# Optimization experiments

Hardware: AMD Instinct MI355X
Metric: run time of the kernel (lower is better)

Reference implementation:

```python
import jax, jax.numpy as jnp
import numpy as np

B, L, H, NH = 4, 512, 512, 8
DK = H // NH
REPR_IN, REPR_HID = 53, 32
EPS = 1e-5


def setup_inputs() -> dict:
    key = jax.random.key(0)
    ks = jax.random.split(key, 12)
    x = jax.random.normal(ks[0], (B, L, H), dtype=jnp.float32)
    mask = jax.random.randint(ks[1], (B, L), 0, 2, dtype=jnp.int32)
    refCov = jax.random.normal(ks[2], (B, L, L, REPR_IN), dtype=jnp.float32)
    def lin(k, fan_in, fan_out):
        return jax.random.normal(k, (fan_in, fan_out), dtype=jnp.float32) / np.sqrt(fan_in)
    Wv = lin(ks[3], H, H); bv = jnp.zeros((H,), jnp.float32)
    W1 = lin(ks[4], REPR_IN, REPR_HID); b1 = jnp.zeros((REPR_HID,), jnp.float32)
    W2 = lin(ks[5], REPR_HID, NH); b2 = jnp.zeros((NH,), jnp.float32)
    Wo = lin(ks[6], H, H); bo = jnp.zeros((H,), jnp.float32)
    gamma = jnp.ones((H,), jnp.float32); beta = jnp.zeros((H,), jnp.float32)
    return {"x": x, "mask": mask, "refCov": refCov, "Wv": Wv, "bv": bv,
            "W1": W1, "b1": b1, "W2": W2, "b2": b2, "Wo": Wo, "bo": bo,
            "gamma": gamma, "beta": beta}


def reference(x, mask, refCov, Wv, bv, W1, b1, W2, b2, Wo, bo, gamma, beta):
    Bx, Lx, Hx = x.shape
    residual = x
    # value projection -> (B, NH, L, DK)
    value = (x @ Wv + bv).reshape(Bx, Lx, NH, DK).transpose(0, 2, 1, 3)
    # per-pair MLP on refCov: (B, L, L, 53) -> (B, L, L, NH)
    h1 = jax.nn.relu(refCov @ W1 + b1)
    scores = jnp.transpose(h1 @ W2 + b2, (0, 3, 1, 2))  # (B, NH, L, L)
    # pairwise mask and softmax
    m = mask.astype(bool)
    mask2d = m[:, :, None] & m[:, None, :]              # (B, L, L)
    masked = jnp.where(mask2d[:, None, :, :], scores, -jnp.inf)
    all_inf_rows = ~jnp.any(mask2d, axis=-1)            # (B, L) rows fully masked
    masked = jnp.where(all_inf_rows[:, None, :, None], 0.0, masked)
    attn = jax.nn.softmax(masked, axis=-1)
    # weighted sum and output projection
    out = jnp.einsum('bhij,bhjd->bhid', attn, value)
    out = out.transpose(0, 2, 1, 3).reshape(Bx, Lx, Hx)
    out = out @ Wo + bo
    # residual + LayerNorm
    y = residual + out
    mu = jnp.mean(y, axis=-1, keepdims=True)
    var = jnp.var(y, axis=-1, keepdims=True)
    return (y - mu) / jnp.sqrt(var + EPS) * gamma + beta
```

## Files before the change

### kernel.cpp

```cpp
#include <hip/hip_runtime.h>
#include <hip/hip_bf16.h>
#include <math.h>

#define B 4
#define L 512
#define H 512
#define NH 8
#define DK 64
#define RIN 53
#define RHID 32

using short8 = __attribute__((ext_vector_type(8))) short;
using ushort8v = __attribute__((ext_vector_type(8))) unsigned short;
using f32x4 = __attribute__((ext_vector_type(4))) float;

__device__ __forceinline__ float waveReduceSum(float v) {
#pragma unroll
  for (int off = 32; off > 0; off >>= 1) v += __shfl_xor(v, off, 64);
  return v;
}

__device__ __forceinline__ unsigned short cvt_bf16(float f) {
  __hip_bfloat16 h = __float2bfloat16(f);
  return __builtin_bit_cast(unsigned short, h);
}

__global__ __launch_bounds__(512) void prep_kernel(
    const int* __restrict__ mask, int* __restrict__ jidx, int* __restrict__ nv,
    const float* __restrict__ Wv, const float* __restrict__ Wo,
    unsigned short* __restrict__ WvT, unsigned short* __restrict__ WoT) {
  const int bid = blockIdx.x;
  const int tid = threadIdx.x;
  if (bid < 4) {
    const int b = bid;
    const int lane = tid & 63, wv = tid >> 6;
    __shared__ int wtot[8], woff[8];
    const int m = (mask[b * 512 + tid] != 0);
    const unsigned long long bal = __ballot(m);
    const int lpre = __popcll(bal & ((1ull << lane) - 1ull));
    if (lane == 0) wtot[wv] = __popcll(bal);
    __syncthreads();
    if (tid == 0) {
      int acc = 0;
#pragma unroll
      for (int q = 0; q < 8; ++q) {
        woff[q] = acc;
        acc += wtot[q];
      }
      nv[b] = acc;
    }
    __syncthreads();
    if (m) jidx[b * 512 + woff[wv] + lpre] = tid;
    return;
  }
  const int t = bid - 4;
  const int matsel = t >> 6;
  const int tile = t & 63;
  const float* W = matsel ? Wo : Wv;
  unsigned short* WT = matsel ? WoT : WvT;
  const int k0 = (tile & 7) * 64, n0 = (tile >> 3) * 64;
  __shared__ float sT[64][65];
  {
    const int r = tid >> 3, c0 = (tid & 7) * 8;
    const float4 v0 = *(const float4*)(W + (size_t)(k0 + r) * 512 + n0 + c0);
    const float4 v1 = *(const float4*)(W + (size_t)(k0 + r) * 512 + n0 + c0 + 4);
    sT[r][c0] = v0.x; sT[r][c0 + 1] = v0.y; sT[r][c0 + 2] = v0.z; sT[r][c0 + 3] = v0.w;
    sT[r][c0 + 4] = v1.x; sT[r][c0 + 5] = v1.y; sT[r][c0 + 6] = v1.z; sT[r][c0 + 7] = v1.w;
  }
  __syncthreads();
  {
    const int n = tid >> 3, c0 = (tid & 7) * 8;
    ushort8v o;
#pragma unroll
    for (int cc = 0; cc < 8; ++cc) o[cc] = cvt_bf16(sT[c0 + cc][n]);
    *(ushort8v*)(WT + (size_t)(n0 + n) * 512 + k0 + c0) = o;
  }
}

template <int AMODE, int OMODE>
__device__ __forceinline__ void gemm32x64(
    const void* __restrict__ Aq, int lda, const unsigned short* __restrict__ Bs,
    int ldb, const float* __restrict__ bias, void* __restrict__ Cp, int ldc) {
  __shared__ unsigned short sA[32 * 72];
  __shared__ unsigned short sB[64 * 72];
  __shared__ float sC[32][68];
  const int tid = threadIdx.x;
  const int w = tid >> 6, l = tid & 63, g = l >> 4, a = l & 15;
  const int wm = (w >> 1) * 16, wn = (w & 1) * 32;
  f32x4 acc0 = {}, acc1 = {};
  const int ar = tid >> 3, ak = (tid & 7) * 8;

  auto loadA = [&](int k0) {
    ushort8v r;
    if constexpr (AMODE == 1) {
      const float* Af = (const float*)Aq;
      const float* p = Af + (size_t)ar * lda + k0 + ak;
      const float4 v0 = *(const float4*)p;
      const float4 v1 = *(const float4*)(p + 4);
      r[0] = cvt_bf16(v0.x); r[1] = cvt_bf16(v0.y);
      r[2] = cvt_bf16(v0.z); r[3] = cvt_bf16(v0.w);
      r[4] = cvt_bf16(v1.x); r[5] = cvt_bf16(v1.y);
      r[6] = cvt_bf16(v1.z); r[7] = cvt_bf16(v1.w);
    } else {
      const unsigned short* Ab = (const unsigned short*)Aq;
      r = *(const ushort8v*)(Ab + (size_t)ar * lda + k0 + ak);
    }
    return r;
  };
  auto loadB = [&](int k0, int q) {
    const int s = tid + q * 256;
    return *(const ushort8v*)(Bs + (size_t)(s >> 3) * ldb + k0 + (s & 7) * 8);
  };

  ushort8v aR = loadA(0);
  ushort8v bR0 = loadB(0, 0), bR1 = loadB(0, 1);
  for (int k0 = 0; k0 < 512; k0 += 64) {
    *(ushort8v*)(&sA[ar * 72 + ak]) = aR;
    *(ushort8v*)(&sB[ar * 72 + ak]) = bR0;
    *(ushort8v*)(&sB[(ar + 32) * 72 + ak]) = bR1;
    __syncthreads();
    if (k0 < 448) {
      aR = loadA(k0 + 64);
      bR0 = loadB(k0 + 64, 0);
      bR1 = loadB(k0 + 64, 1);
    }
#pragma unroll
    for (int ks = 0; ks < 2; ++ks) {
      const short8 af = *(const short8*)(&sA[(wm + a) * 72 + ks * 32 + g * 8]);
      const short8 bf0 = *(const short8*)(&sB[(wn + a) * 72 + ks * 32 + g * 8]);
      const short8 bf1 =
          *(const short8*)(&sB[(wn + 16 + a) * 72 + ks * 32 + g * 8]);
      acc0 = __builtin_amdgcn_mfma_f32_16x16x32_bf16(af, bf0, acc0, 0, 0, 0);
      acc1 = __builtin_amdgcn_mfma_f32_16x16x32_bf16(af, bf1, acc1, 0, 0, 0);
    }
    __syncthreads();
  }

#pragma unroll
  for (int r = 0; r < 4; ++r) {
    sC[wm + g * 4 + r][wn + a] = acc0[r];
    sC[wm + g * 4 + r][wn + 16 + a] = acc1[r];
  }
  __syncthreads();

  if constexpr (OMODE == 2) {
    const int n = tid >> 2, iq = (tid & 3) * 8;
    const float bv = bias ? bias[n] : 0.f;
    ushort8v o;
#pragma unroll
    for (int cc = 0; cc < 8; ++cc) o[cc] = cvt_bf16(sC[iq + cc][n] + bv);
    *(ushort8v*)((unsigned short*)Cp + (size_t)n * ldc + iq) = o;
  } else {
    const int m = tid >> 3, c8 = (tid & 7) * 8;
    float v[8];
#pragma unroll
    for (int cc = 0; cc < 8; ++cc) {
      v[cc] = sC[m][c8 + cc];
      if (bias) v[cc] += bias[c8 + cc];
    }
    if constexpr (OMODE == 1) {
      ushort8v o;
#pragma unroll
      for (int cc = 0; cc < 8; ++cc) o[cc] = cvt_bf16(v[cc]);
      *(ushort8v*)((unsigned short*)Cp + (size_t)m * ldc + c8) = o;
    } else {
      *(float4*)((float*)Cp + (size_t)m * ldc + c8) =
          make_float4(v[0], v[1], v[2], v[3]);
      *(float4*)((float*)Cp + (size_t)m * ldc + c8 + 4) =
          make_float4(v[4], v[5], v[6], v[7]);
    }
  }
}

__global__ __launch_bounds__(256) void gemm_xw_t_kernel(
    const float* __restrict__ x, const unsigned short* __restrict__ WvT,
    const float* __restrict__ bv, unsigned short* __restrict__ valT) {
  const int n0 = blockIdx.x * 64;
  const int m0 = blockIdx.y * 32;
  const int b = m0 >> 9, i0 = m0 & 511;
  gemm32x64<1, 2>(x + (size_t)m0 * 512, 512, WvT + (size_t)n0 * 512, 512,
                  bv + n0, valT + (size_t)b * 262144 + (size_t)n0 * 512 + i0,
                  512);
}

__global__ __launch_bounds__(256) void attn_value_kernel(
    const unsigned short* __restrict__ attnb,
    const unsigned short* __restrict__ valT, unsigned short* __restrict__ ctx) {
  const int bid = blockIdx.x;
  const int it = bid & 15, h = (bid >> 4) & 7, b = bid >> 7;
  const int i0 = it * 32;
  gemm32x64<0, 1>(attnb + ((size_t)((b * 8 + h) * 512 + i0)) * 512, 512,
                  valT + (size_t)b * 262144 + (size_t)(h * 64) * 512, 512,
                  nullptr, ctx + ((size_t)(b * 512 + i0)) * 512 + h * 64, 512);
}

__global__ __launch_bounds__(256) void gemm_proj_kernel(
    const unsigned short* __restrict__ ctx, const unsigned short* __restrict__ WoT,
    const float* __restrict__ bo, float* __restrict__ proj) {
  const int n0 = blockIdx.x * 64;
  const int m0 = blockIdx.y * 32;
  gemm32x64<0, 0>(ctx + (size_t)m0 * 512, 512, WoT + (size_t)n0 * 512, 512,
                  bo + n0, proj + (size_t)m0 * 512 + n0, 512);
}

__global__ __launch_bounds__(256) void residual_ln_kernel(
    const float* __restrict__ x, const float* __restrict__ proj,
    const float* __restrict__ gamma, const float* __restrict__ beta,
    float* __restrict__ out) {
  const int row = blockIdx.x;
  const int tid = threadIdx.x;
  __shared__ float redS[4], redQ[4];
  float y[2];
  float ls = 0.f, lq = 0.f;
#pragma unroll
  for (int p = 0; p < 2; ++p) {
    const int c = tid + p * 256;
    const float v = x[(size_t)row * H + c] + proj[(size_t)row * H + c];
    y[p] = v;
    ls += v;
    lq += v * v;
  }
  const int lane = tid & 63, wave = tid >> 6;
  ls = waveReduceSum(ls);
  lq = waveReduceSum(lq);
  if (lane == 0) {
    redS[wave] = ls;
    redQ[wave] = lq;
  }
  __syncthreads();
  const float sum = redS[0] + redS[1] + redS[2] + redS[3];
  const float sq = redQ[0] + redQ[1] + redQ[2] + redQ[3];
  const float mu = sum * (1.f / H);
  const float var = sq * (1.f / H) - mu * mu;
  const float inv = rsqrtf(var + 1e-5f);
#pragma unroll
  for (int p = 0; p < 2; ++p) {
    const int c = tid + p * 256;
    out[(size_t)row * H + c] = (y[p] - mu) * inv * gamma[c] + beta[c];
  }
}

__global__ __launch_bounds__(256) void scores_softmax_kernel(
    const float* __restrict__ refCov, const int* __restrict__ mask,
    const int* __restrict__ jidx, const int* __restrict__ nvArr,
    const float* __restrict__ W1, const float* __restrict__ b1,
    const float* __restrict__ W2, const float* __restrict__ b2,
    unsigned short* __restrict__ attnb) {
  __shared__ unsigned short sH1[512 * 34];
  __shared__ int sJ[512];
  __shared__ float redbuf[4][16];

  const int tid = threadIdx.x;
  const int b = blockIdx.x >> 9;
  const int i = blockIdx.x & (L - 1);
  const int w = tid >> 6;
  const int l = tid & 63;
  const int g = l >> 4;
  const int a = l & 15;

  const int mi = mask[b * L + i];
  const int nv = nvArr[b];

  if (mi == 0 || nv == 0) {
    const ushort4 u4 = {0x3B00u, 0x3B00u, 0x3B00u, 0x3B00u};
#pragma unroll
    for (int q = 0; q < 4; ++q) {
      const int f4 = q * 256 + tid;
      const int h = f4 >> 7;
      const int c4 = f4 & 127;
      *(ushort4*)(attnb + ((size_t)(b * NH + h) * L + i) * L + c4 * 4) = u4;
    }
    return;
  }

  sJ[tid] = jidx[b * 512 + tid];
  sJ[tid + 256] = jidx[b * 512 + 256 + tid];

  short8 w1f[2][2];
#pragma unroll
  for (int ks = 0; ks < 2; ++ks)
#pragma unroll
    for (int nt = 0; nt < 2; ++nt)
#pragma unroll
      for (int e = 0; e < 8; ++e) {
        const int k = ks * 32 + g * 8 + e;
        w1f[ks][nt][e] =
            (k < RIN) ? (short)cvt_bf16(W1[k * RHID + nt * 16 + a]) : (short)0;
      }
  short8 w2f;
#pragma unroll
  for (int e = 0; e < 8; ++e) {
    const int k = g * 8 + e;
    w2f[e] = (a < NH) ? (short)cvt_bf16(W2[k * NH + a]) : (short)0;
  }
  const float b1v0 = b1[a];
  const float b1v1 = b1[16 + a];
  const float b2v = (a < NH) ? b2[a] : 0.f;

  __syncthreads();

  const int NT = (nv + 15) >> 4;
  f32x4 sc[8];

#pragma unroll
  for (int mt = 0; mt < 8; ++mt) {
    const int t = mt * 4 + w;
    if (t >= NT) continue;
    const int s = t * 16 + a;
    const int j = sJ[(s < nv) ? s : (nv - 1)];
    const float* rp = refCov + ((size_t)((b << 9) + i) * 512 + j) * RIN;

    const float4 u0 = *(const float4*)(rp + g * 8);
    const float4 u1 = *(const float4*)(rp + g * 8 + 4);
    const int base0 = (g < 3) ? (32 + g * 8) : 32;
    const int base1 = (g == 0) ? 36 : (g == 1) ? 44 : 49;
    const float4 v0 = *(const float4*)(rp + base0);
    const float4 v1 = *(const float4*)(rp + base1);
    float t1[8];
    if (g < 3) {
      t1[0] = v0.x; t1[1] = v0.y; t1[2] = v0.z; t1[3] = v0.w;
    } else {
      t1[0] = 0.f; t1[1] = 0.f; t1[2] = 0.f; t1[3] = 0.f;
    }
    if (g < 2) {
      t1[4] = v1.x; t1[5] = v1.y; t1[6] = v1.z; t1[7] = v1.w;
    } else if (g == 2) {
      t1[4] = v1.w;
      t1[5] = 0.f; t1[6] = 0.f; t1[7] = 0.f;
    } else {
      t1[4] = 0.f; t1[5] = 0.f; t1[6] = 0.f; t1[7] = 0.f;
    }
    short8 af0, af1;
    af0[0] = (short)cvt_bf16(u0.x); af0[1] = (short)cvt_bf16(u0.y);
    af0[2] = (short)cvt_bf16(u0.z); af0[3] = (short)cvt_bf16(u0.w);
    af0[4] = (short)cvt_bf16(u1.x); af0[5] = (short)cvt_bf16(u1.y);
    af0[6] = (short)cvt_bf16(u1.z); af0[7] = (short)cvt_bf16(u1.w);
#pragma unroll
    for (int e = 0; e < 8; ++e) af1[e] = (short)cvt_bf16(t1[e]);

    f32x4 h0 = f32x4{b1v0, b1v0, b1v0, b1v0};
    f32x4 h1v = f32x4{b1v1, b1v1, b1v1, b1v1};
    h0 = __builtin_amdgcn_mfma_f32_16x16x32_bf16(af0, w1f[0][0], h0, 0, 0, 0);
    h1v = __builtin_amdgcn_mfma_f32_16x16x32_bf16(af0, w1f[0][1], h1v, 0, 0, 0);
    h0 = __builtin_amdgcn_mfma_f32_16x16x32_bf16(af1, w1f[1][0], h0, 0, 0, 0);
    h1v = __builtin_amdgcn_mfma_f32_16x16x32_bf16(af1, w1f[1][1], h1v, 0, 0, 0);

#pragma unroll
    for (int r = 0; r < 4; ++r) {
      sH1[(t * 16 + g * 4 + r) * 34 + a] = cvt_bf16(fmaxf(h0[r], 0.f));
      sH1[(t * 16 + g * 4 + r) * 34 + 16 + a] = cvt_bf16(fmaxf(h1v[r], 0.f));
    }

    const short8 af2 = *(const short8*)(&sH1[(t * 16 + a) * 34 + g * 8]);
    f32x4 acc = f32x4{b2v, b2v, b2v, b2v};
    sc[mt] = __builtin_amdgcn_mfma_f32_16x16x32_bf16(af2, w2f, acc, 0, 0, 0);
  }

  float mx = -INFINITY;
#pragma unroll
  for (int mt = 0; mt < 8; ++mt) {
    const int t = mt * 4 + w;
    if (t >= NT) continue;
#pragma unroll
    for (int r = 0; r < 4; ++r) {
      const int s = t * 16 + g * 4 + r;
      if (s < nv) mx = fmaxf(mx, sc[mt][r]);
    }
  }
  mx = fmaxf(mx, __shfl_xor(mx, 16, 64));
  mx = fmaxf(mx, __shfl_xor(mx, 32, 64));
  if (g == 0) redbuf[w][a] = mx;
  __syncthreads();
  const float rmax = fmaxf(fmaxf(redbuf[0][a], redbuf[1][a]),
                           fmaxf(redbuf[2][a], redbuf[3][a]));
  __syncthreads();

  float lsum = 0.f;
#pragma unroll
  for (int mt = 0; mt < 8; ++mt) {
    const int t = mt * 4 + w;
    if (t >= NT) continue;
#pragma unroll
    for (int r = 0; r < 4; ++r) {
      const int s = t * 16 + g * 4 + r;
      const float e = (s < nv) ? __expf(sc[mt][r] - rmax) : 0.f;
      sc[mt][r] = e;
      lsum += e;
    }
  }
  lsum += __shfl_xor(lsum, 16, 64);
  lsum += __shfl_xor(lsum, 32, 64);
  if (g == 0) redbuf[w][a] = lsum;
  __syncthreads();
  const float rsum = redbuf[0][a] + redbuf[1][a] + redbuf[2][a] + redbuf[3][a];
  const float inv = 1.f / rsum;

  unsigned short* sOut = sH1;
  __syncthreads();
  {
    const ushort8v z{};
    *(ushort8v*)(&sOut[tid * 16]) = z;
    *(ushort8v*)(&sOut[tid * 16 + 8]) = z;
  }
  __syncthreads();
  if (a < NH) {
#pragma unroll
    for (int mt = 0; mt < 8; ++mt) {
      const int t = mt * 4 + w;
      if (t >= NT) continue;
#pragma unroll
      for (int r = 0; r < 4; ++r) {
        const int s = t * 16 + g * 4 + r;
        if (s < nv) sOut[a * 512 + sJ[s]] = cvt_bf16(sc[mt][r] * inv);
      }
    }
  }
  __syncthreads();
  {
    const int h = tid >> 5, off = (tid & 31) * 16;
    unsigned short* dst = attnb + ((size_t)(b * NH + h) * L + i) * L + off;
    *(ushort8v*)dst = *(const ushort8v*)(&sOut[h * 512 + off]);
    *(ushort8v*)(dst + 8) = *(const ushort8v*)(&sOut[h * 512 + off + 8]);
  }
}

extern "C" void kernel_launch(void* const* d_in, const int* in_sizes, int n_in,
                              void* d_out, int out_size, void* d_ws,
                              size_t ws_size, hipStream_t stream) {
  const float* x = (const float*)d_in[0];
  const int* mask = (const int*)d_in[1];
  const float* refCov = (const float*)d_in[2];
  const float* Wv = (const float*)d_in[3];
  const float* bv = (const float*)d_in[4];
  const float* W1 = (const float*)d_in[5];
  const float* b1 = (const float*)d_in[6];
  const float* W2 = (const float*)d_in[7];
  const float* b2 = (const float*)d_in[8];
  const float* Wo = (const float*)d_in[9];
  const float* bo = (const float*)d_in[10];
  const float* gamma = (const float*)d_in[11];
  const float* beta = (const float*)d_in[12];
  float* out = (float*)d_out;

  const size_t n_attn = (size_t)B * NH * L * L;
  const size_t n_blh = (size_t)B * L * H;
  const size_t n_w = (size_t)H * H;
  unsigned short* attnb = (unsigned short*)d_ws;
  unsigned short* valT = attnb + n_attn;
  unsigned short* ctx = valT + n_blh;
  unsigned short* WvT = ctx + n_blh;
  unsigned short* WoT = WvT + n_w;
  float* proj = (float*)(WoT + n_w);
  int* jidx = (int*)(proj + n_blh);
  int* nv = jidx + B * L;
  const size_t needed =
      (n_attn + 2 * n_blh + 2 * n_w) * 2 + n_blh * 4 + (B * L + B) * 4;
  if (ws_size < needed) return;

  const int M = B * L;

  prep_kernel<<<132, 512, 0, stream>>>(mask, jidx, nv, Wv, Wo, WvT, WoT);
  gemm_xw_t_kernel<<<dim3(8, M / 32), 256, 0, stream>>>(x, WvT, bv, valT);
  scores_softmax_kernel<<<B * L, 256, 0, stream>>>(refCov, mask, jidx, nv, W1,
                                                   b1, W2, b2, attnb);
  attn_value_kernel<<<512, 256, 0, stream>>>(attnb, valT, ctx);
  gemm_proj_kernel<<<dim3(8, M / 32), 256, 0, stream>>>(ctx, WoT, bo, proj);
  residual_ln_kernel<<<M, 256, 0, stream>>>(x, proj, gamma, beta, out);
}
```

Baseline: 65.69 us.

## Merge value projection GEMM into scores-softmax launch and shrink shared memory

New measurement: 61.06 us. 1.08x faster.

```diff
diff --git a/kernel.cpp b/kernel.cpp
--- a/kernel.cpp
+++ b/kernel.cpp
@@ -77,13 +77,15 @@
   }
 }
 
+#define GEMM_SMEM 13824
 template <int AMODE, int OMODE>
 __device__ __forceinline__ void gemm32x64(
-    const void* __restrict__ Aq, int lda, const unsigned short* __restrict__ Bs,
-    int ldb, const float* __restrict__ bias, void* __restrict__ Cp, int ldc) {
-  __shared__ unsigned short sA[32 * 72];
-  __shared__ unsigned short sB[64 * 72];
-  __shared__ float sC[32][68];
+    char* __restrict__ smem, const void* __restrict__ Aq, int lda,
+    const unsigned short* __restrict__ Bs, int ldb,
+    const float* __restrict__ bias, void* __restrict__ Cp, int ldc) {
+  unsigned short* sA = (unsigned short*)smem;
+  unsigned short* sB = (unsigned short*)(smem + 4608);
+  float(*sC)[68] = (float(*)[68])smem;
   const int tid = threadIdx.x;
   const int w = tid >> 6, l = tid & 63, g = l >> 4, a = l & 15;
   const int wm = (w >> 1) * 16, wn = (w & 1) * 32;
@@ -172,85 +174,34 @@
   }
 }
 
-__global__ __launch_bounds__(256) void gemm_xw_t_kernel(
-    const float* __restrict__ x, const unsigned short* __restrict__ WvT,
-    const float* __restrict__ bv, unsigned short* __restrict__ valT) {
-  const int n0 = blockIdx.x * 64;
-  const int m0 = blockIdx.y * 32;
-  const int b = m0 >> 9, i0 = m0 & 511;
-  gemm32x64<1, 2>(x + (size_t)m0 * 512, 512, WvT + (size_t)n0 * 512, 512,
-                  bv + n0, valT + (size_t)b * 262144 + (size_t)n0 * 512 + i0,
-                  512);
-}
-
-__global__ __launch_bounds__(256) void attn_value_kernel(
-    const unsigned short* __restrict__ attnb,
-    const unsigned short* __restrict__ valT, unsigned short* __restrict__ ctx) {
-  const int bid = blockIdx.x;
-  const int it = bid & 15, h = (bid >> 4) & 7, b = bid >> 7;
-  const int i0 = it * 32;
-  gemm32x64<0, 1>(attnb + ((size_t)((b * 8 + h) * 512 + i0)) * 512, 512,
-                  valT + (size_t)b * 262144 + (size_t)(h * 64) * 512, 512,
-                  nullptr, ctx + ((size_t)(b * 512 + i0)) * 512 + h * 64, 512);
-}
-
-__global__ __launch_bounds__(256) void gemm_proj_kernel(
-    const unsigned short* __restrict__ ctx, const unsigned short* __restrict__ WoT,
-    const float* __restrict__ bo, float* __restrict__ proj) {
-  const int n0 = blockIdx.x * 64;
-  const int m0 = blockIdx.y * 32;
-  gemm32x64<0, 0>(ctx + (size_t)m0 * 512, 512, WoT + (size_t)n0 * 512, 512,
-                  bo + n0, proj + (size_t)m0 * 512 + n0, 512);
-}
-
-__global__ __launch_bounds__(256) void residual_ln_kernel(
-    const float* __restrict__ x, const float* __restrict__ proj,
-    const float* __restrict__ gamma, const float* __restrict__ beta,
-    float* __restrict__ out) {
-  const int row = blockIdx.x;
-  const int tid = threadIdx.x;
-  __shared__ float redS[4], redQ[4];
-  float y[2];
-  float ls = 0.f, lq = 0.f;
-#pragma unroll
-  for (int p = 0; p < 2; ++p) {
-    const int c = tid + p * 256;
-    const float v = x[(size_t)row * H + c] + proj[(size_t)row * H + c];
-    y[p] = v;
-    ls += v;
-    lq += v * v;
-  }
-  const int lane = tid & 63, wave = tid >> 6;
-  ls = waveReduceSum(ls);
-  lq = waveReduceSum(lq);
-  if (lane == 0) {
-    redS[wave] = ls;
-    redQ[wave] = lq;
-  }
-  __syncthreads();
-  const float sum = redS[0] + redS[1] + redS[2] + redS[3];
-  const float sq = redQ[0] + redQ[1] + redQ[2] + redQ[3];
-  const float mu = sum * (1.f / H);
-  const float var = sq * (1.f / H) - mu * mu;
-  const float inv = rsqrtf(var + 1e-5f);
-#pragma unroll
-  for (int p = 0; p < 2; ++p) {
-    const int c = tid + p * 256;
-    out[(size_t)row * H + c] = (y[p] - mu) * inv * gamma[c] + beta[c];
-  }
-}
-
-__global__ __launch_bounds__(256) void scores_softmax_kernel(
+#define FUSED_SMEM 15616
+__global__ __launch_bounds__(256) void fused_scores_value_kernel(
     const float* __restrict__ refCov, const int* __restrict__ mask,
     const int* __restrict__ jidx, const int* __restrict__ nvArr,
     const float* __restrict__ W1, const float* __restrict__ b1,
     const float* __restrict__ W2, const float* __restrict__ b2,
-    unsigned short* __restrict__ attnb) {
-  __shared__ unsigned short sH1[512 * 34];
-  __shared__ int sJ[512];
-  __shared__ float redbuf[4][16];
-
+    unsigned short* __restrict__ attnb, const float* __restrict__ x,
+    const unsigned short* __restrict__ WvT, const float* __restrict__ bv,
+    unsigned short* __restrict__ valT) {
+  __shared__ __align__(16) char smem[FUSED_SMEM];
   const int tid = threadIdx.x;
+
+  if (blockIdx.x >= 2048) {
+    const int gb = blockIdx.x - 2048;
+    const int n0 = (gb & 7) * 64;
+    const int m0 = (gb >> 3) * 32;
+    const int b = m0 >> 9, i0 = m0 & 511;
+    gemm32x64<1, 2>(smem, x + (size_t)m0 * 512, 512, WvT + (size_t)n0 * 512,
+                    512, bv + n0,
+                    valT + (size_t)b * 262144 + (size_t)n0 * 512 + i0, 512);
+    return;
+  }
+
+  unsigned short* sH1 = (unsigned short*)smem;
+  int* sJ = (int*)(smem + 5120);
+  unsigned short* sOut = (unsigned short*)(smem + 7168);
+  float(*redbuf)[16] = (float(*)[16])(smem + 15360);
+
   const int b = blockIdx.x >> 9;
   const int i = blockIdx.x & (L - 1);
   const int w = tid >> 6;
@@ -347,11 +298,11 @@
 
 #pragma unroll
     for (int r = 0; r < 4; ++r) {
-      sH1[(t * 16 + g * 4 + r) * 34 + a] = cvt_bf16(fmaxf(h0[r], 0.f));
-      sH1[(t * 16 + g * 4 + r) * 34 + 16 + a] = cvt_bf16(fmaxf(h1v[r], 0.f));
-    }
-
-    const short8 af2 = *(const short8*)(&sH1[(t * 16 + a) * 34 + g * 8]);
+      sH1[(w * 16 + g * 4 + r) * 40 + a] = cvt_bf16(fmaxf(h0[r], 0.f));
+      sH1[(w * 16 + g * 4 + r) * 40 + 16 + a] = cvt_bf16(fmaxf(h1v[r], 0.f));
+    }
+
+    const short8 af2 = *(const short8*)(&sH1[(w * 16 + a) * 40 + g * 8]);
     f32x4 acc = f32x4{b2v, b2v, b2v, b2v};
     sc[mt] = __builtin_amdgcn_mfma_f32_16x16x32_bf16(af2, w2f, acc, 0, 0, 0);
   }
@@ -395,8 +346,6 @@
   const float rsum = redbuf[0][a] + redbuf[1][a] + redbuf[2][a] + redbuf[3][a];
   const float inv = 1.f / rsum;
 
-  unsigned short* sOut = sH1;
-  __syncthreads();
   {
     const ushort8v z{};
     *(ushort8v*)(&sOut[tid * 16]) = z;
@@ -421,6 +370,66 @@
     unsigned short* dst = attnb + ((size_t)(b * NH + h) * L + i) * L + off;
     *(ushort8v*)dst = *(const ushort8v*)(&sOut[h * 512 + off]);
     *(ushort8v*)(dst + 8) = *(const ushort8v*)(&sOut[h * 512 + off + 8]);
+  }
+}
+
+__global__ __launch_bounds__(256) void attn_value_kernel(
+    const unsigned short* __restrict__ attnb,
+    const unsigned short* __restrict__ valT, unsigned short* __restrict__ ctx) {
+  __shared__ __align__(16) char smem[GEMM_SMEM];
+  const int bid = blockIdx.x;
+  const int it = bid & 15, h = (bid >> 4) & 7, b = bid >> 7;
+  const int i0 = it * 32;
+  gemm32x64<0, 1>(smem, attnb + ((size_t)((b * 8 + h) * 512 + i0)) * 512, 512,
+                  valT + (size_t)b * 262144 + (size_t)(h * 64) * 512, 512,
+                  nullptr, ctx + ((size_t)(b * 512 + i0)) * 512 + h * 64, 512);
+}
+
+__global__ __launch_bounds__(256) void gemm_proj_kernel(
+    const unsigned short* __restrict__ ctx,
+    const unsigned short* __restrict__ WoT, const float* __restrict__ bo,
+    float* __restrict__ proj) {
+  __shared__ __align__(16) char smem[GEMM_SMEM];
+  const int n0 = blockIdx.x * 64;
+  const int m0 = blockIdx.y * 32;
+  gemm32x64<0, 0>(smem, ctx + (size_t)m0 * 512, 512, WoT + (size_t)n0 * 512,
+                  512, bo + n0, proj + (size_t)m0 * 512 + n0, 512);
+}
+
+__global__ __launch_bounds__(256) void residual_ln_kernel(
+    const float* __restrict__ x, const float* __restrict__ proj,
+    const float* __restrict__ gamma, const float* __restrict__ beta,
+    float* __restrict__ out) {
+  const int row = blockIdx.x;
+  const int tid = threadIdx.x;
+  __shared__ float redS[4], redQ[4];
+  float y[2];
+  float ls = 0.f, lq = 0.f;
+#pragma unroll
+  for (int p = 0; p < 2; ++p) {
+    const int c = tid + p * 256;
+    const float v = x[(size_t)row * H + c] + proj[(size_t)row * H + c];
+    y[p] = v;
+    ls += v;
+    lq += v * v;
+  }
+  const int lane = tid & 63, wave = tid >> 6;
+  ls = waveReduceSum(ls);
+  lq = waveReduceSum(lq);
+  if (lane == 0) {
+    redS[wave] = ls;
+    redQ[wave] = lq;
+  }
+  __syncthreads();
+  const float sum = redS[0] + redS[1] + redS[2] + redS[3];
+  const float sq = redQ[0] + redQ[1] + redQ[2] + redQ[3];
+  const float mu = sum * (1.f / H);
+  const float var = sq * (1.f / H) - mu * mu;
+  const float inv = rsqrtf(var + 1e-5f);
+#pragma unroll
+  for (int p = 0; p < 2; ++p) {
+    const int c = tid + p * 256;
+    out[(size_t)row * H + c] = (y[p] - mu) * inv * gamma[c] + beta[c];
   }
 }
 
@@ -460,9 +469,8 @@
   const int M = B * L;
 
   prep_kernel<<<132, 512, 0, stream>>>(mask, jidx, nv, Wv, Wo, WvT, WoT);
-  gemm_xw_t_kernel<<<dim3(8, M / 32), 256, 0, stream>>>(x, WvT, bv, valT);
-  scores_softmax_kernel<<<B * L, 256, 0, stream>>>(refCov, mask, jidx, nv, W1,
-                                                   b1, W2, b2, attnb);
+  fused_scores_value_kernel<<<2048 + 512, 256, 0, stream>>>(
+      refCov, mask, jidx, nv, W1, b1, W2, b2, attnb, x, WvT, bv, valT);
   attn_value_kernel<<<512, 256, 0, stream>>>(attnb, valT, ctx);
   gemm_proj_kernel<<<dim3(8, M / 32), 256, 0, stream>>>(ctx, WoT, bo, proj);
   residual_ln_kernel<<<M, 256, 0, stream>>>(x, proj, gamma, beta, out);
```
